# Kernel tuning notes

Measured on AMD Instinct MI355X. Metric: run time of the kernel, lower is better.

Reference implementation:

```python
import jax, jax.numpy as jnp
import numpy as np

EPS = 1e-12  # matches torch F.normalize default


def _l2norm_c(x):
    # normalize along channel dim (axis=1) of [B,C,H,W]
    n = jnp.sqrt(jnp.sum(x * x, axis=1, keepdims=True))
    return x / jnp.maximum(n, EPS)


def setup_inputs() -> dict:
    key = jax.random.key(0)
    ks = jax.random.split(key, 6)
    B, C, H, W = 2, 256, 64, 64
    return {
        "sv": jax.random.normal(ks[0], (B, 1, H, W), dtype=jnp.float32),
        "si": jax.random.normal(ks[1], (B, 1, H, W), dtype=jnp.float32),
        "sf": jax.random.normal(ks[2], (B, 1, H, W), dtype=jnp.float32),
        "dv": jax.random.normal(ks[3], (B, C, H, W), dtype=jnp.float32),
        "di": jax.random.normal(ks[4], (B, C, H, W), dtype=jnp.float32),
        "df": jax.random.normal(ks[5], (B, C, H, W), dtype=jnp.float32),
    }


def reference(sv, si, sf, dv, di, df):
    # keypoint score loss: L1(sf, max(sv, si))
    kp = jnp.mean(jnp.abs(sf - jnp.maximum(sv, si)))
    # descriptor loss: L1(df, (dv+di)/2)
    desc = jnp.mean(jnp.abs(df - (dv + di) * 0.5))
    # match loss (dense): normalize along C, full correlation volumes, L1
    a = _l2norm_c(dv)
    b = _l2norm_c(di)
    c = _l2norm_c(df)
    sim_ab = jnp.einsum('bchw,bcij->bhwij', a, b)  # [B,H,W,H,W]
    sim_ac = jnp.einsum('bchw,bcij->bhwij', a, c)
    match = jnp.mean(jnp.abs(sim_ac - sim_ab))
    return kp + desc + match
```

## Files before the change

### kernel.cpp

```cpp
#include <hip/hip_runtime.h>
#include <hip/hip_bf16.h>
#include <math.h>

#define BB 2
#define CC 256
#define CCP (CC + 2)
#define HWN 4096
#define PT 32
#define NBLK (32 * 32 * BB)


typedef __attribute__((ext_vector_type(4))) int   intx4;
typedef __attribute__((ext_vector_type(8))) int   intx8;
typedef __attribute__((ext_vector_type(4))) float floatx4;

__device__ __forceinline__ unsigned short f2bf(float f) {
    union { float f; unsigned u; } v; v.f = f;
    unsigned r = v.u + 0x7FFF + ((v.u >> 16) & 1);
    return (unsigned short)(r >> 16);
}

__device__ __forceinline__ float bf2f(unsigned short h) {
    union { unsigned u; float f; } v; v.u = ((unsigned)h) << 16;
    return v.f;
}

__global__ __launch_bounds__(1024) void prep_kernel(
    const float* __restrict__ sv, const float* __restrict__ si,
    const float* __restrict__ sf, const float* __restrict__ dv,
    const float* __restrict__ di, const float* __restrict__ df,
    unsigned char* __restrict__ Af8, unsigned char* __restrict__ Df8,
    float* __restrict__ pk, float* __restrict__ pd)
{
    __shared__ unsigned short lv[PT][CCP];
    __shared__ unsigned short li[PT][CCP];
    __shared__ unsigned short lf[PT][CCP];
    __shared__ float ssq[3][PT];
    __shared__ float inv[3][PT];
    __shared__ float sdesc;

    const int b   = blockIdx.x / (HWN / PT);
    const int p0  = (blockIdx.x % (HWN / PT)) * PT;
    const int tid = threadIdx.x;
    const int tp4 = tid & 7;
    const int c0  = (tid >> 3) * 2;

    if (tid < 3 * PT) ((float*)ssq)[tid] = 0.0f;
    if (tid == 0) sdesc = 0.0f;
    __syncthreads();

    const size_t rbase = ((size_t)b * CC + c0) * HWN + p0 + tp4 * 4;
    const floatx4 v0 = *(const floatx4*)(dv + rbase);
    const floatx4 v1 = *(const floatx4*)(dv + rbase + HWN);
    const floatx4 i0 = *(const floatx4*)(di + rbase);
    const floatx4 i1 = *(const floatx4*)(di + rbase + HWN);
    const floatx4 f0 = *(const floatx4*)(df + rbase);
    const floatx4 f1 = *(const floatx4*)(df + rbase + HWN);

    float sqv[4], sqi[4], sqf[4], descp = 0.f;
    #pragma unroll
    for (int k = 0; k < 4; ++k) {
        sqv[k] = v0[k] * v0[k] + v1[k] * v1[k];
        sqi[k] = i0[k] * i0[k] + i1[k] * i1[k];
        sqf[k] = f0[k] * f0[k] + f1[k] * f1[k];
        descp += fabsf(f0[k] - 0.5f * (v0[k] + i0[k]))
               + fabsf(f1[k] - 0.5f * (v1[k] + i1[k]));
        const int p = tp4 * 4 + k;
        *(unsigned*)&lv[p][c0] = (unsigned)f2bf(v0[k]) | ((unsigned)f2bf(v1[k]) << 16);
        *(unsigned*)&li[p][c0] = (unsigned)f2bf(i0[k]) | ((unsigned)f2bf(i1[k]) << 16);
        *(unsigned*)&lf[p][c0] = (unsigned)f2bf(f0[k]) | ((unsigned)f2bf(f1[k]) << 16);
    }

    #pragma unroll
    for (int off = 8; off < 64; off <<= 1) {
        #pragma unroll
        for (int k = 0; k < 4; ++k) {
            sqv[k] += __shfl_down(sqv[k], off);
            sqi[k] += __shfl_down(sqi[k], off);
            sqf[k] += __shfl_down(sqf[k], off);
        }
    }
    if ((tid & 63) < 8) {
        #pragma unroll
        for (int k = 0; k < 4; ++k) {
            atomicAdd(&ssq[0][tp4 * 4 + k], sqv[k]);
            atomicAdd(&ssq[1][tp4 * 4 + k], sqi[k]);
            atomicAdd(&ssq[2][tp4 * 4 + k], sqf[k]);
        }
    }

    #pragma unroll
    for (int off = 32; off > 0; off >>= 1) descp += __shfl_down(descp, off);
    if ((tid & 63) == 0) atomicAdd(&sdesc, descp);

    if (tid < 64) {
        float kpv = 0.f;
        if (tid < PT) {
            const size_t sidx = (size_t)b * HWN + p0 + tid;
            kpv = fabsf(sf[sidx] - fmaxf(sv[sidx], si[sidx]));
        }
        #pragma unroll
        for (int off = 32; off > 0; off >>= 1) kpv += __shfl_down(kpv, off);
        if (tid == 0) pk[blockIdx.x] = kpv;
    }
    __syncthreads();

    if (tid < 3 * PT) {
        const float s = ((float*)ssq)[tid];
        ((float*)inv)[tid] = 1.0f / fmaxf(sqrtf(s), 1e-12f);
    }
    __syncthreads();

    if (tid == 0) pd[blockIdx.x] = sdesc;

    int* Ao = (int*)(Af8 + (size_t)b * HWN * CC);
    int* Do = (int*)(Df8 + (size_t)b * HWN * CC);
    #pragma unroll
    for (int i = tid; i < PT * CC / 4; i += 1024) {
        const int p = i >> 6, cc0 = (i & 63) * 4;
        const int P = p0 + p;
        const int oidx = (P >> 4) * 1024 + (cc0 >> 5) * 128 + (P & 15) * 8
                       + ((cc0 & 31) >> 2);
        const float ia = inv[0][p], ib = inv[1][p], ic = inv[2][p];
        float a0 = bf2f(lv[p][cc0 + 0]) * ia, a1 = bf2f(lv[p][cc0 + 1]) * ia;
        float a2 = bf2f(lv[p][cc0 + 2]) * ia, a3 = bf2f(lv[p][cc0 + 3]) * ia;
        float d0 = bf2f(lf[p][cc0 + 0]) * ic - bf2f(li[p][cc0 + 0]) * ib;
        float d1 = bf2f(lf[p][cc0 + 1]) * ic - bf2f(li[p][cc0 + 1]) * ib;
        float d2 = bf2f(lf[p][cc0 + 2]) * ic - bf2f(li[p][cc0 + 2]) * ib;
        float d3 = bf2f(lf[p][cc0 + 3]) * ic - bf2f(li[p][cc0 + 3]) * ib;
        int wa = __builtin_amdgcn_cvt_pk_fp8_f32(a0, a1, 0, false);
        wa     = __builtin_amdgcn_cvt_pk_fp8_f32(a2, a3, wa, true);
        int wd = __builtin_amdgcn_cvt_pk_fp8_f32(d0, d1, 0, false);
        wd     = __builtin_amdgcn_cvt_pk_fp8_f32(d2, d3, wd, true);
        Ao[oidx] = wa;
        Do[oidx] = wd;
    }
}

__global__ __launch_bounds__(256) void gemm_abs_kernel(
    const unsigned char* __restrict__ Af8,
    const unsigned char* __restrict__ Df8,
    float* __restrict__ pg)
{
    const int b    = blockIdx.z;
    const int tid  = threadIdx.x;
    const int wave = tid >> 6;
    const int lane = tid & 63;
    const int wr   = wave >> 1, wc = wave & 1;
    const int mg0  = blockIdx.x * 8 + wr * 4;
    const int ng0  = blockIdx.y * 8 + wc * 4;

    const unsigned char* Ab = Af8 + (size_t)b * HWN * CC;
    const unsigned char* Db = Df8 + (size_t)b * HWN * CC;
    const int lofs = (lane >> 4) * 512 + (lane & 15) * 32;

    intx4 a[4][2][2], bb[4][2][2];
    #pragma unroll
    for (int mi = 0; mi < 4; ++mi)
        #pragma unroll
        for (int ks = 0; ks < 2; ++ks) {
            const unsigned char* pa = Ab + (size_t)(mg0 + mi) * 4096
                                    + ks * 2048 + lofs;
            a[mi][ks][0] = *(const intx4*)(pa);
            a[mi][ks][1] = *(const intx4*)(pa + 16);
        }
    #pragma unroll
    for (int ni = 0; ni < 4; ++ni)
        #pragma unroll
        for (int ks = 0; ks < 2; ++ks) {
            const unsigned char* pb = Db + (size_t)(ng0 + ni) * 4096
                                    + ks * 2048 + lofs;
            bb[ni][ks][0] = *(const intx4*)(pb);
            bb[ni][ks][1] = *(const intx4*)(pb + 16);
        }

    floatx4 accf[4][4];
    #pragma unroll
    for (int mi = 0; mi < 4; ++mi)
        #pragma unroll
        for (int ni = 0; ni < 4; ++ni)
            accf[mi][ni] = (floatx4){0.f, 0.f, 0.f, 0.f};

    #pragma unroll
    for (int ks = 0; ks < 2; ++ks)
        #pragma unroll
        for (int mi = 0; mi < 4; ++mi) {
            const intx8 a8 = __builtin_shufflevector(
                a[mi][ks][0], a[mi][ks][1], 0, 1, 2, 3, 4, 5, 6, 7);
            #pragma unroll
            for (int ni = 0; ni < 4; ++ni) {
                const intx8 b8 = __builtin_shufflevector(
                    bb[ni][ks][0], bb[ni][ks][1], 0, 1, 2, 3, 4, 5, 6, 7);
                accf[mi][ni] = __builtin_amdgcn_mfma_scale_f32_16x16x128_f8f6f4(
                    a8, b8, accf[mi][ni],
                    0, 0,
                    0, 0x7F7F7F7F,
                    0, 0x7F7F7F7F);
            }
        }

    float s = 0.f;
    #pragma unroll
    for (int mi = 0; mi < 4; ++mi)
        #pragma unroll
        for (int ni = 0; ni < 4; ++ni)
            #pragma unroll
            for (int r = 0; r < 4; ++r)
                s += fabsf(accf[mi][ni][r]);
    #pragma unroll
    for (int off = 32; off > 0; off >>= 1) s += __shfl_down(s, off);
    if (lane == 0) {
        const int flat = blockIdx.x + 32 * (blockIdx.y + 32 * blockIdx.z);
        pg[flat * 4 + wave] = s;
    }
}

__global__ __launch_bounds__(256) void final_kernel(
    const float* __restrict__ pg, const float* __restrict__ pk,
    const float* __restrict__ pd, float* __restrict__ out)
{
    __shared__ float ws[4];
    const int t = threadIdx.x;
    float s = 0.f;
    #pragma unroll
    for (int i = 0; i < 32; ++i)
        s += pg[t + i * 256];
    s *= (1.0f / 33554432.0f);
    s += pk[t] * (1.0f / 8192.0f)
       + pd[t] * (1.0f / 2097152.0f);
    #pragma unroll
    for (int off = 32; off > 0; off >>= 1) s += __shfl_down(s, off);
    if ((t & 63) == 0) ws[t >> 6] = s;
    __syncthreads();
    if (t == 0) out[0] = ws[0] + ws[1] + ws[2] + ws[3];
}

extern "C" void kernel_launch(void* const* d_in, const int* in_sizes, int n_in,
                              void* d_out, int out_size, void* d_ws, size_t ws_size,
                              hipStream_t stream) {
    const float* sv = (const float*)d_in[0];
    const float* si = (const float*)d_in[1];
    const float* sf = (const float*)d_in[2];
    const float* dv = (const float*)d_in[3];
    const float* di = (const float*)d_in[4];
    const float* df = (const float*)d_in[5];

    unsigned char* Af8 = (unsigned char*)d_ws;
    unsigned char* Df8 = Af8 + (size_t)BB * HWN * CC;
    float* pg = (float*)(Df8 + (size_t)BB * HWN * CC);
    float* pk = pg + 8192;
    float* pd = pk + 256;

    prep_kernel<<<dim3(BB * (HWN / PT)), 1024, 0, stream>>>(
        sv, si, sf, dv, di, df, Af8, Df8, pk, pd);
    gemm_abs_kernel<<<dim3(HWN / 128, HWN / 128, BB), 256, 0, stream>>>(
        Af8, Df8, pg);
    final_kernel<<<1, 256, 0, stream>>>(pg, pk, pd, (float*)d_out);
}
```

Baseline: 98.01 us.

## Split prep into norm and separate fp8 pack kernel reading inputs directly

The fused prep kernel is split in two. A norm kernel computes per-pixel inverse norms, writes them to a global buffer, and also produces the keypoint and descriptor partial sums. A new pack kernel re-reads dv/di/df from global memory, scales them by the stored inverse norms, and writes the fp8 A and D tiles. This drops the bf16 LDS staging and its extra rounding step, and may improve occupancy. The cost is a second full pass over the three 8 MB inputs, an extra kernel launch, and narrow 32-byte strided loads in the pack kernel.

```diff
diff --git a/kernel.cpp b/kernel.cpp
--- a/kernel.cpp
+++ b/kernel.cpp
@@ -4,39 +4,22 @@
 
 #define BB 2
 #define CC 256
-#define CCP (CC + 2)
 #define HWN 4096
 #define PT 32
-#define NBLK (32 * 32 * BB)
 
 
 typedef __attribute__((ext_vector_type(4))) int   intx4;
 typedef __attribute__((ext_vector_type(8))) int   intx8;
 typedef __attribute__((ext_vector_type(4))) float floatx4;
 
-__device__ __forceinline__ unsigned short f2bf(float f) {
-    union { float f; unsigned u; } v; v.f = f;
-    unsigned r = v.u + 0x7FFF + ((v.u >> 16) & 1);
-    return (unsigned short)(r >> 16);
-}
-
-__device__ __forceinline__ float bf2f(unsigned short h) {
-    union { unsigned u; float f; } v; v.u = ((unsigned)h) << 16;
-    return v.f;
-}
-
-__global__ __launch_bounds__(1024) void prep_kernel(
+__global__ __launch_bounds__(1024) void norm_kernel(
     const float* __restrict__ sv, const float* __restrict__ si,
     const float* __restrict__ sf, const float* __restrict__ dv,
     const float* __restrict__ di, const float* __restrict__ df,
-    unsigned char* __restrict__ Af8, unsigned char* __restrict__ Df8,
-    float* __restrict__ pk, float* __restrict__ pd)
-{
-    __shared__ unsigned short lv[PT][CCP];
-    __shared__ unsigned short li[PT][CCP];
-    __shared__ unsigned short lf[PT][CCP];
+    float* __restrict__ invn, float* __restrict__ pk,
+    float* __restrict__ pd)
+{
     __shared__ float ssq[3][PT];
-    __shared__ float inv[3][PT];
     __shared__ float sdesc;
 
     const int b   = blockIdx.x / (HWN / PT);
@@ -65,10 +48,6 @@
         sqf[k] = f0[k] * f0[k] + f1[k] * f1[k];
         descp += fabsf(f0[k] - 0.5f * (v0[k] + i0[k]))
                + fabsf(f1[k] - 0.5f * (v1[k] + i1[k]));
-        const int p = tp4 * 4 + k;
-        *(unsigned*)&lv[p][c0] = (unsigned)f2bf(v0[k]) | ((unsigned)f2bf(v1[k]) << 16);
-        *(unsigned*)&li[p][c0] = (unsigned)f2bf(i0[k]) | ((unsigned)f2bf(i1[k]) << 16);
-        *(unsigned*)&lf[p][c0] = (unsigned)f2bf(f0[k]) | ((unsigned)f2bf(f1[k]) << 16);
     }
 
     #pragma unroll
@@ -106,32 +85,55 @@
     __syncthreads();
 
     if (tid < 3 * PT) {
+        const int t = tid >> 5, p = tid & 31;
         const float s = ((float*)ssq)[tid];
-        ((float*)inv)[tid] = 1.0f / fmaxf(sqrtf(s), 1e-12f);
-    }
-    __syncthreads();
-
+        invn[t * (BB * HWN) + b * HWN + p0 + p] =
+            1.0f / fmaxf(sqrtf(s), 1e-12f);
+    }
     if (tid == 0) pd[blockIdx.x] = sdesc;
-
+}
+
+__global__ __launch_bounds__(256) void pack_kernel(
+    const float* __restrict__ dv, const float* __restrict__ di,
+    const float* __restrict__ df, const float* __restrict__ invn,
+    unsigned char* __restrict__ Af8, unsigned char* __restrict__ Df8)
+{
+    const int pg0  = blockIdx.x * 16;
+    const int h    = blockIdx.y;
+    const int b    = blockIdx.z;
+    const int tid  = threadIdx.x;
+    const int wave = tid >> 6;
+    const int lane = tid & 63;
+    const int kb   = h * 4 + wave;
+    const int cg   = lane & 7;
+    const int pr   = lane >> 3;
+
+    const int c0 = kb * 32 + cg * 4;
+    const float* dvb = dv + ((size_t)b * CC + c0) * HWN;
+    const float* dib = di + ((size_t)b * CC + c0) * HWN;
+    const float* dfb = df + ((size_t)b * CC + c0) * HWN;
     int* Ao = (int*)(Af8 + (size_t)b * HWN * CC);
     int* Do = (int*)(Df8 + (size_t)b * HWN * CC);
-    #pragma unroll
-    for (int i = tid; i < PT * CC / 4; i += 1024) {
-        const int p = i >> 6, cc0 = (i & 63) * 4;
-        const int P = p0 + p;
-        const int oidx = (P >> 4) * 1024 + (cc0 >> 5) * 128 + (P & 15) * 8
-                       + ((cc0 & 31) >> 2);
-        const float ia = inv[0][p], ib = inv[1][p], ic = inv[2][p];
-        float a0 = bf2f(lv[p][cc0 + 0]) * ia, a1 = bf2f(lv[p][cc0 + 1]) * ia;
-        float a2 = bf2f(lv[p][cc0 + 2]) * ia, a3 = bf2f(lv[p][cc0 + 3]) * ia;
-        float d0 = bf2f(lf[p][cc0 + 0]) * ic - bf2f(li[p][cc0 + 0]) * ib;
-        float d1 = bf2f(lf[p][cc0 + 1]) * ic - bf2f(li[p][cc0 + 1]) * ib;
-        float d2 = bf2f(lf[p][cc0 + 2]) * ic - bf2f(li[p][cc0 + 2]) * ib;
-        float d3 = bf2f(lf[p][cc0 + 3]) * ic - bf2f(li[p][cc0 + 3]) * ib;
-        int wa = __builtin_amdgcn_cvt_pk_fp8_f32(a0, a1, 0, false);
-        wa     = __builtin_amdgcn_cvt_pk_fp8_f32(a2, a3, wa, true);
-        int wd = __builtin_amdgcn_cvt_pk_fp8_f32(d0, d1, 0, false);
-        wd     = __builtin_amdgcn_cvt_pk_fp8_f32(d2, d3, wd, true);
+    const int obase = (pg0 >> 4) * 1024 + kb * 128;
+
+    #pragma unroll
+    for (int s = 0; s < 2; ++s) {
+        const int P = pg0 + pr + s * 8;
+        const float ia = invn[0 * (BB * HWN) + b * HWN + P];
+        const float ib = invn[1 * (BB * HWN) + b * HWN + P];
+        const float ic = invn[2 * (BB * HWN) + b * HWN + P];
+        float a[4], d[4];
+        #pragma unroll
+        for (int j = 0; j < 4; ++j) {
+            const size_t idx = (size_t)j * HWN + P;
+            a[j] = dvb[idx] * ia;
+            d[j] = dfb[idx] * ic - dib[idx] * ib;
+        }
+        int wa = __builtin_amdgcn_cvt_pk_fp8_f32(a[0], a[1], 0, false);
+        wa     = __builtin_amdgcn_cvt_pk_fp8_f32(a[2], a[3], wa, true);
+        int wd = __builtin_amdgcn_cvt_pk_fp8_f32(d[0], d[1], 0, false);
+        wd     = __builtin_amdgcn_cvt_pk_fp8_f32(d[2], d[3], wd, true);
+        const int oidx = obase + (pr + s * 8) * 8 + cg;
         Ao[oidx] = wa;
         Do[oidx] = wd;
     }
@@ -247,12 +249,15 @@
 
     unsigned char* Af8 = (unsigned char*)d_ws;
     unsigned char* Df8 = Af8 + (size_t)BB * HWN * CC;
-    float* pg = (float*)(Df8 + (size_t)BB * HWN * CC);
-    float* pk = pg + 8192;
-    float* pd = pk + 256;
-
-    prep_kernel<<<dim3(BB * (HWN / PT)), 1024, 0, stream>>>(
-        sv, si, sf, dv, di, df, Af8, Df8, pk, pd);
+    float* pg   = (float*)(Df8 + (size_t)BB * HWN * CC);
+    float* pk   = pg + 8192;
+    float* pd   = pk + 256;
+    float* invn = pd + 256;
+
+    norm_kernel<<<dim3(BB * (HWN / PT)), 1024, 0, stream>>>(
+        sv, si, sf, dv, di, df, invn, pk, pd);
+    pack_kernel<<<dim3(HWN / 16, 2, BB), 256, 0, stream>>>(
+        dv, di, df, invn, Af8, Df8);
     gemm_abs_kernel<<<dim3(HWN / 128, HWN / 128, BB), 256, 0, stream>>>(
         Af8, Df8, pg);
     final_kernel<<<1, 256, 0, stream>>>(pg, pk, pd, (float*)d_out);
```

Measured after the change: 106.0 us. +8.2%, slower.
